# Optimization experiments

Hardware: AMD Instinct MI355X
Metric: run time of the kernel (lower is better)

## Reference

```python
import jax, jax.numpy as jnp
import numpy as np
from jax import lax

ALIVE_THRESHOLD = 0.1
GROWTH_BOOST = 1.0  # forward default arg

_SX = jnp.array([[-1., 0., 1.], [-2., 0., 2.], [-1., 0., 1.]], dtype=jnp.float32)
_SY = jnp.array([[-1., -2., -1.], [0., 0., 0.], [1., 2., 1.]], dtype=jnp.float32)


def _depthwise3x3(x, k):
    # x: [B,C,H,W], k: [3,3] -> depthwise conv, padding 1 (SAME)
    C = x.shape[1]
    w = jnp.tile(k[None, None], (C, 1, 1, 1))  # [C,1,3,3]
    return lax.conv_general_dilated(
        x, w, window_strides=(1, 1), padding='SAME',
        dimension_numbers=('NCHW', 'OIHW', 'NCHW'), feature_group_count=C)


def _avg_pool3x3(x):
    # torch avg_pool2d(k=3, stride=1, pad=1, count_include_pad=True) == sum window / 9 with zero pad
    w = jnp.ones((1, 1, 3, 3), dtype=x.dtype) / 9.0
    return lax.conv_general_dilated(
        x, w, window_strides=(1, 1), padding='SAME',
        dimension_numbers=('NCHW', 'OIHW', 'NCHW'))


def setup_inputs() -> dict:
    key = jax.random.key(0)
    ks = jax.random.split(key, 5)
    B, C, H, W = 16, 8, 512, 512
    x = jax.random.normal(ks[0], (B, C, H, W), dtype=jnp.float32)
    # kaiming_normal_(a=0.3) -> std = sqrt(2/(1+a^2)) / sqrt(fan_in)
    gain = float(np.sqrt(2.0 / (1.0 + 0.3 ** 2)))
    w1 = jax.random.normal(ks[1], (32, 24), dtype=jnp.float32) * (gain / np.sqrt(24))
    w2 = jax.random.normal(ks[2], (32, 32), dtype=jnp.float32) * (gain / np.sqrt(32))
    w3 = jax.random.normal(ks[3], (8, 32), dtype=jnp.float32) * (gain / np.sqrt(32))
    b1 = jnp.full((32,), 0.05, dtype=jnp.float32)
    b2 = jnp.full((32,), 0.05, dtype=jnp.float32)
    b3 = jnp.full((8,), 0.05, dtype=jnp.float32)
    growth_rate = jnp.array([0.3], dtype=jnp.float32)
    return {'x': x, 'w1': w1, 'b1': b1, 'w2': w2, 'b2': b2,
            'w3': w3, 'b3': b3, 'growth_rate': growth_rate}


def reference(x, w1, b1, w2, b2, w3, b3, growth_rate):
    # perceive: [x, sobel_x(x), sobel_y(x)] -> [B, 3C, H, W]
    perceived = jnp.concatenate([x, _depthwise3x3(x, _SX), _depthwise3x3(x, _SY)], axis=1)
    # per-pixel MLP (1x1 convs)
    h = jax.nn.relu(jnp.einsum('bchw,oc->bohw', perceived, w1) + b1[None, :, None, None])
    h = jax.nn.relu(jnp.einsum('bchw,oc->bohw', h, w2) + b2[None, :, None, None])
    dx = jnp.einsum('bchw,oc->bohw', h, w3) + b3[None, :, None, None]
    dx = dx * growth_rate[0] * GROWTH_BOOST
    # alive masking / growth zones
    alive_mask = (x[:, 3:4] > ALIVE_THRESHOLD).astype(x.dtype)
    alive_ratio = jnp.mean(alive_mask)
    neighbor_alive = _avg_pool3x3(alive_mask)
    growth_zones = (neighbor_alive > 0.01).astype(x.dtype) * 0.2  # [B,1,H,W]
    boost = jnp.where(alive_ratio < 0.2, growth_zones, jnp.zeros_like(growth_zones))
    dx = jnp.concatenate([dx[:, :3], dx[:, 3:4] + boost, dx[:, 4:]], axis=1)
    new_x = jnp.clip(x + dx, -1.0, 1.0)
    alpha = jnp.clip(new_x[:, 3:4], 0.0, 1.0)
    return jnp.concatenate([new_x[:, :3], alpha, new_x[:, 4:]], axis=1)
```

## Files before the change

kernel.cpp:

```cpp
#include <hip/hip_runtime.h>

namespace {

constexpr int kH = 512, kW = 512, kB = 16, kC = 8;
constexpr int kHW = kH * kW;
constexpr int kBS = kC * kHW;
constexpr int TW = 64, TH = 4;
constexpr int TWP = TW + 2, THP = TH + 2;

__global__ __launch_bounds__(256)
void alive_count_kernel(const float* __restrict__ x, int* __restrict__ cnt) {
    __shared__ int sdata[4];
    const int tid = threadIdx.x;
    const int total4 = kB * kHW / 4;
    int idx = blockIdx.x * 256 + tid;
    const int stride = gridDim.x * 256;
    int local = 0;
    const float4* x4 = (const float4*)x;
    for (int i = idx; i < total4; i += stride) {
        int b = i >> 16;
        int off = i & 65535;
        float4 v = x4[(size_t)b * (kBS / 4) + (3 * kHW / 4) + off];
        local += (v.x > 0.1f) + (v.y > 0.1f) + (v.z > 0.1f) + (v.w > 0.1f);
    }
    for (int off = 32; off > 0; off >>= 1)
        local += __shfl_down(local, off, 64);
    if ((tid & 63) == 0) sdata[tid >> 6] = local;
    __syncthreads();
    if (tid == 0) atomicAdd(cnt, sdata[0] + sdata[1] + sdata[2] + sdata[3]);
}

__global__ __launch_bounds__(256, 2)
void nca_fused_kernel(const float* __restrict__ x,
                      const float* __restrict__ w1, const float* __restrict__ b1,
                      const float* __restrict__ w2, const float* __restrict__ b2,
                      const float* __restrict__ w3, const float* __restrict__ b3,
                      const float* __restrict__ growth,
                      const int* __restrict__ alive_cnt,
                      float* __restrict__ out) {
    __shared__ float tile[kC][THP][TWP];

    const int w0 = blockIdx.x * TW;
    const int h0 = blockIdx.y * TH;
    const int b  = blockIdx.z;
    const int tid = threadIdx.x;
    const float* xb = x + b * kBS;

    constexpr int TILE_N = kC * THP * TWP;
    for (int i = tid; i < TILE_N; i += 256) {
        int c  = i / (THP * TWP);
        int r  = i - c * (THP * TWP);
        int hh = r / TWP;
        int ww = r - hh * TWP;
        int gh = h0 + hh - 1;
        int gw = w0 + ww - 1;
        float v = 0.0f;
        if ((unsigned)gh < (unsigned)kH && (unsigned)gw < (unsigned)kW)
            v = xb[c * kHW + gh * kW + gw];
        (&tile[0][0][0])[i] = v;
    }
    __syncthreads();

    const int ww = tid & (TW - 1);
    const int hh = tid >> 6;

    float p[24];
    int nalive = 0;
#pragma unroll
    for (int c = 0; c < kC; ++c) {
        float a00 = tile[c][hh    ][ww], a01 = tile[c][hh    ][ww + 1], a02 = tile[c][hh    ][ww + 2];
        float a10 = tile[c][hh + 1][ww], a11 = tile[c][hh + 1][ww + 1], a12 = tile[c][hh + 1][ww + 2];
        float a20 = tile[c][hh + 2][ww], a21 = tile[c][hh + 2][ww + 1], a22 = tile[c][hh + 2][ww + 2];
        p[c]      = a11;
        p[8 + c]  = (a02 - a00) + 2.0f * (a12 - a10) + (a22 - a20);
        p[16 + c] = (a20 - a00) + 2.0f * (a21 - a01) + (a22 - a02);
        if (c == 3) {
            nalive = (a00 > 0.1f) + (a01 > 0.1f) + (a02 > 0.1f)
                   + (a10 > 0.1f) + (a11 > 0.1f) + (a12 > 0.1f)
                   + (a20 > 0.1f) + (a21 > 0.1f) + (a22 > 0.1f);
        }
    }

    float h1[32];
#pragma unroll
    for (int o = 0; o < 32; ++o) {
        float acc = b1[o];
#pragma unroll
        for (int i2 = 0; i2 < 24; ++i2) acc = fmaf(w1[o * 24 + i2], p[i2], acc);
        h1[o] = fmaxf(acc, 0.0f);
    }
    float h2[32];
#pragma unroll
    for (int o = 0; o < 32; ++o) {
        float acc = b2[o];
#pragma unroll
        for (int i2 = 0; i2 < 32; ++i2) acc = fmaf(w2[o * 32 + i2], h1[i2], acc);
        h2[o] = fmaxf(acc, 0.0f);
    }
    float d[8];
#pragma unroll
    for (int o = 0; o < 8; ++o) {
        float acc = b3[o];
#pragma unroll
        for (int i2 = 0; i2 < 32; ++i2) acc = fmaf(w3[o * 32 + i2], h2[i2], acc);
        d[o] = acc;
    }

    const float g = growth[0];
    const float ratio = (float)(*alive_cnt) * (1.0f / 4194304.0f);
    const float boost = (ratio < 0.2f && nalive > 0) ? 0.2f : 0.0f;

    float* ob = out + b * kBS + (h0 + hh) * kW + (w0 + ww);
#pragma unroll
    for (int c = 0; c < kC; ++c) {
        float v = p[c] + d[c] * g + ((c == 3) ? boost : 0.0f);
        const float lo = (c == 3) ? 0.0f : -1.0f;
        v = fminf(fmaxf(v, lo), 1.0f);
        ob[c * kHW] = v;
    }
}

}

extern "C" void kernel_launch(void* const* d_in, const int* in_sizes, int n_in,
                              void* d_out, int out_size, void* d_ws, size_t ws_size,
                              hipStream_t stream) {
    const float* x  = (const float*)d_in[0];
    const float* w1 = (const float*)d_in[1];
    const float* b1 = (const float*)d_in[2];
    const float* w2 = (const float*)d_in[3];
    const float* b2 = (const float*)d_in[4];
    const float* w3 = (const float*)d_in[5];
    const float* b3 = (const float*)d_in[6];
    const float* gr = (const float*)d_in[7];
    float* out = (float*)d_out;
    int* cnt = (int*)d_ws;

    hipMemsetAsync(cnt, 0, sizeof(int), stream);
    alive_count_kernel<<<256, 256, 0, stream>>>(x, cnt);
    dim3 grid(kW / TW, kH / TH, kB);
    nca_fused_kernel<<<grid, 256, 0, stream>>>(x, w1, b1, w2, b2, w3, b3, gr, cnt, out);
}
```

Baseline: 474.5 us.

## Run per-pixel MLP on MFMA f16 matrix cores via shared-memory staging

Replaces the scalar fp32 per-pixel 24→32→32→8 MLP with MFMA 16x16x32 f16 instructions. Each wave stages its 64 pixels' perception features into an XOR-swizzled shared scratch buffer and reuses it for the hidden activations between layers. Weights are held as f16 fragments in registers and biases are folded into the accumulator init. It also raises the launch-bounds occupancy hint from 2 to 3 blocks. This removes the large FMA count per pixel but adds LDS round trips and f16 rounding of activations and dx, which may affect accuracy.

```diff
diff --git a/kernel.cpp b/kernel.cpp
--- a/kernel.cpp
+++ b/kernel.cpp
@@ -1,12 +1,17 @@
 #include <hip/hip_runtime.h>
 
 namespace {
+
+using h16x8 = __attribute__((ext_vector_type(8))) _Float16;
+using h16x4 = __attribute__((ext_vector_type(4))) _Float16;
+using f32x4 = __attribute__((ext_vector_type(4))) float;
 
 constexpr int kH = 512, kW = 512, kB = 16, kC = 8;
 constexpr int kHW = kH * kW;
 constexpr int kBS = kC * kHW;
 constexpr int TW = 64, TH = 4;
 constexpr int TWP = TW + 2, THP = TH + 2;
+constexpr int SS = 40;
 
 __global__ __launch_bounds__(256)
 void alive_count_kernel(const float* __restrict__ x, int* __restrict__ cnt) {
@@ -30,7 +35,7 @@
     if (tid == 0) atomicAdd(cnt, sdata[0] + sdata[1] + sdata[2] + sdata[3]);
 }
 
-__global__ __launch_bounds__(256, 2)
+__global__ __launch_bounds__(256, 3)
 void nca_fused_kernel(const float* __restrict__ x,
                       const float* __restrict__ w1, const float* __restrict__ b1,
                       const float* __restrict__ w2, const float* __restrict__ b2,
@@ -39,12 +44,43 @@
                       const int* __restrict__ alive_cnt,
                       float* __restrict__ out) {
     __shared__ float tile[kC][THP][TWP];
+    __shared__ __align__(16) _Float16 scr[4][64 * SS];
 
     const int w0 = blockIdx.x * TW;
     const int h0 = blockIdx.y * TH;
     const int b  = blockIdx.z;
     const int tid = threadIdx.x;
-    const float* xb = x + b * kBS;
+    const int wv = tid >> 6;
+    const int ln = tid & 63;
+    const int lm = ln & 15;
+    const int lq = ln >> 4;
+    const float* xb = x + (size_t)b * kBS;
+    _Float16* base = scr[wv];
+
+    h16x8 w1f[2], w2f[2], w3f;
+#pragma unroll
+    for (int mi = 0; mi < 2; ++mi) {
+        int m = mi * 16 + lm;
+#pragma unroll
+        for (int j = 0; j < 8; ++j) {
+            int k = lq * 8 + j;
+            w1f[mi][j] = (k < 24) ? (_Float16)w1[m * 24 + k] : (_Float16)0.0f;
+            w2f[mi][j] = (_Float16)w2[m * 32 + k];
+        }
+    }
+#pragma unroll
+    for (int j = 0; j < 8; ++j)
+        w3f[j] = (lm < 8) ? (_Float16)w3[lm * 32 + lq * 8 + j] : (_Float16)0.0f;
+
+    f32x4 bias1[2], bias2[2], bias3;
+#pragma unroll
+    for (int mi = 0; mi < 2; ++mi) {
+        int m0 = mi * 16 + lq * 4;
+#pragma unroll
+        for (int r = 0; r < 4; ++r) { bias1[mi][r] = b1[m0 + r]; bias2[mi][r] = b2[m0 + r]; }
+    }
+#pragma unroll
+    for (int r = 0; r < 4; ++r) bias3[r] = (lq < 2) ? b3[lq * 4 + r] : 0.0f;
 
     constexpr int TILE_N = kC * THP * TWP;
     for (int i = tid; i < TILE_N; i += 256) {
@@ -61,19 +97,18 @@
     }
     __syncthreads();
 
-    const int ww = tid & (TW - 1);
-    const int hh = tid >> 6;
-
-    float p[24];
+    float pc[8];
+    h16x8 vx, vsx, vsy;
     int nalive = 0;
 #pragma unroll
     for (int c = 0; c < kC; ++c) {
-        float a00 = tile[c][hh    ][ww], a01 = tile[c][hh    ][ww + 1], a02 = tile[c][hh    ][ww + 2];
-        float a10 = tile[c][hh + 1][ww], a11 = tile[c][hh + 1][ww + 1], a12 = tile[c][hh + 1][ww + 2];
-        float a20 = tile[c][hh + 2][ww], a21 = tile[c][hh + 2][ww + 1], a22 = tile[c][hh + 2][ww + 2];
-        p[c]      = a11;
-        p[8 + c]  = (a02 - a00) + 2.0f * (a12 - a10) + (a22 - a20);
-        p[16 + c] = (a20 - a00) + 2.0f * (a21 - a01) + (a22 - a02);
+        float a00 = tile[c][wv    ][ln], a01 = tile[c][wv    ][ln + 1], a02 = tile[c][wv    ][ln + 2];
+        float a10 = tile[c][wv + 1][ln], a11 = tile[c][wv + 1][ln + 1], a12 = tile[c][wv + 1][ln + 2];
+        float a20 = tile[c][wv + 2][ln], a21 = tile[c][wv + 2][ln + 1], a22 = tile[c][wv + 2][ln + 2];
+        pc[c]  = a11;
+        vx[c]  = (_Float16)a11;
+        vsx[c] = (_Float16)((a02 - a00) + 2.0f * (a12 - a10) + (a22 - a20));
+        vsy[c] = (_Float16)((a20 - a00) + 2.0f * (a21 - a01) + (a22 - a02));
         if (c == 3) {
             nalive = (a00 > 0.1f) + (a01 > 0.1f) + (a02 > 0.1f)
                    + (a10 > 0.1f) + (a11 > 0.1f) + (a12 > 0.1f)
@@ -81,39 +116,94 @@
         }
     }
 
-    float h1[32];
-#pragma unroll
-    for (int o = 0; o < 32; ++o) {
-        float acc = b1[o];
-#pragma unroll
-        for (int i2 = 0; i2 < 24; ++i2) acc = fmaf(w1[o * 24 + i2], p[i2], acc);
-        h1[o] = fmaxf(acc, 0.0f);
-    }
-    float h2[32];
-#pragma unroll
-    for (int o = 0; o < 32; ++o) {
-        float acc = b2[o];
-#pragma unroll
-        for (int i2 = 0; i2 < 32; ++i2) acc = fmaf(w2[o * 32 + i2], h1[i2], acc);
-        h2[o] = fmaxf(acc, 0.0f);
-    }
-    float d[8];
-#pragma unroll
-    for (int o = 0; o < 8; ++o) {
-        float acc = b3[o];
-#pragma unroll
-        for (int i2 = 0; i2 < 32; ++i2) acc = fmaf(w3[o * 32 + i2], h2[i2], acc);
-        d[o] = acc;
-    }
+    {
+        const int sw = (ln >> 2) & 3;
+        *(h16x8*)(base + ln * SS + (0 ^ sw) * 8) = vx;
+        *(h16x8*)(base + ln * SS + (1 ^ sw) * 8) = vsx;
+        *(h16x8*)(base + ln * SS + (2 ^ sw) * 8) = vsy;
+        h16x8 z = {};
+        *(h16x8*)(base + ln * SS + (3 ^ sw) * 8) = z;
+    }
+
+    auto readB = [&](int ni) -> h16x8 {
+        int row = ni * 16 + lm;
+        int phys = lq ^ ((row >> 2) & 3);
+        return *(const h16x8*)(base + row * SS + phys * 8);
+    };
+    auto writeH = [&](int mi, int ni, f32x4 h) {
+        int row = ni * 16 + lm;
+        int cl = mi * 2 + (lq >> 1);
+        int phys = cl ^ ((row >> 2) & 3);
+        h16x4 v;
+#pragma unroll
+        for (int r = 0; r < 4; ++r) v[r] = (_Float16)h[r];
+        *(h16x4*)(base + row * SS + phys * 8 + (lq & 1) * 4) = v;
+    };
+
+    h16x8 bfr[4];
+    f32x4 acc[2][4];
+
+#pragma unroll
+    for (int ni = 0; ni < 4; ++ni) bfr[ni] = readB(ni);
+#pragma unroll
+    for (int ni = 0; ni < 4; ++ni)
+#pragma unroll
+        for (int mi = 0; mi < 2; ++mi)
+            acc[mi][ni] = __builtin_amdgcn_mfma_f32_16x16x32_f16(w1f[mi], bfr[ni], bias1[mi], 0, 0, 0);
+#pragma unroll
+    for (int mi = 0; mi < 2; ++mi)
+#pragma unroll
+        for (int ni = 0; ni < 4; ++ni) {
+            f32x4 h = acc[mi][ni];
+#pragma unroll
+            for (int r = 0; r < 4; ++r) h[r] = fmaxf(h[r], 0.0f);
+            writeH(mi, ni, h);
+        }
+
+#pragma unroll
+    for (int ni = 0; ni < 4; ++ni) bfr[ni] = readB(ni);
+#pragma unroll
+    for (int ni = 0; ni < 4; ++ni)
+#pragma unroll
+        for (int mi = 0; mi < 2; ++mi)
+            acc[mi][ni] = __builtin_amdgcn_mfma_f32_16x16x32_f16(w2f[mi], bfr[ni], bias2[mi], 0, 0, 0);
+#pragma unroll
+    for (int mi = 0; mi < 2; ++mi)
+#pragma unroll
+        for (int ni = 0; ni < 4; ++ni) {
+            f32x4 h = acc[mi][ni];
+#pragma unroll
+            for (int r = 0; r < 4; ++r) h[r] = fmaxf(h[r], 0.0f);
+            writeH(mi, ni, h);
+        }
+
+    f32x4 acc3[4];
+#pragma unroll
+    for (int ni = 0; ni < 4; ++ni) bfr[ni] = readB(ni);
+#pragma unroll
+    for (int ni = 0; ni < 4; ++ni)
+        acc3[ni] = __builtin_amdgcn_mfma_f32_16x16x32_f16(w3f, bfr[ni], bias3, 0, 0, 0);
 
     const float g = growth[0];
     const float ratio = (float)(*alive_cnt) * (1.0f / 4194304.0f);
     const float boost = (ratio < 0.2f && nalive > 0) ? 0.2f : 0.0f;
 
-    float* ob = out + b * kBS + (h0 + hh) * kW + (w0 + ww);
-#pragma unroll
-    for (int c = 0; c < kC; ++c) {
-        float v = p[c] + d[c] * g + ((c == 3) ? boost : 0.0f);
+    if (lq < 2) {
+#pragma unroll
+        for (int ni = 0; ni < 4; ++ni) {
+            int row = ni * 16 + lm;
+            h16x4 v;
+#pragma unroll
+            for (int r = 0; r < 4; ++r) v[r] = (_Float16)(acc3[ni][r] * g);
+            *(h16x4*)(base + row * SS + 32 + lq * 4) = v;
+        }
+    }
+    h16x8 dxv = *(const h16x8*)(base + ln * SS + 32);
+
+    float* ob = out + (size_t)b * kBS + (h0 + wv) * kW + (w0 + ln);
+#pragma unroll
+    for (int c = 0; c < 8; ++c) {
+        float v = pc[c] + (float)dxv[c] + ((c == 3) ? boost : 0.0f);
         const float lo = (c == 3) ? 0.0f : -1.0f;
         v = fminf(fmaxf(v, lo), 1.0f);
         ob[c * kHW] = v;
```

Measured after the change: 536.5 us. 13.1% more time.
